# Kernel tuning notes

Hardware: AMD Instinct MI355X
Metric: run time of the kernel (lower is better)

## Reference

```python
import jax, jax.numpy as jnp
import numpy as np

B, NTH, NTW, M, DF = 64, 56, 56, 8, 8
FAR = 100.0  # sentinel location for off sources, as in the torch module


def setup_inputs() -> dict:
    key = jax.random.key(0)
    k1, k2, k3, k4, k5 = jax.random.split(key, 5)
    est_locs = jax.random.uniform(k1, (B, NTH, NTW, M, 2), dtype=jnp.float32)
    true_locs = jax.random.uniform(k2, (B, NTH, NTW, M, 2), dtype=jnp.float32)
    true_fluxes = jax.random.normal(k3, (B, NTH, NTW, M, DF), dtype=jnp.float32)
    est_n_sources = jax.random.randint(k4, (B, NTH, NTW), 0, M + 1, dtype=jnp.int32)
    true_n_sources = jax.random.randint(k5, (B, NTH, NTW), 0, M + 1, dtype=jnp.int32)
    return {"est_locs": est_locs, "true_locs": true_locs, "true_fluxes": true_fluxes,
            "est_n_sources": est_n_sources, "true_n_sources": true_n_sources}


def reference(est_locs, true_locs, true_fluxes, est_n_sources, true_n_sources):
    b, nth, ntw, m, _ = est_locs.shape
    T = b * nth * ntw
    slot = jnp.arange(m)
    # is_on_mask per tile: first n_sources slots are on
    est_on = slot[None, :] < est_n_sources.reshape(T, 1)    # [T, m] bool
    true_on = slot[None, :] < true_n_sources.reshape(T, 1)  # [T, m] bool

    # masked locs -> pairwise L2 distances (torch.cdist p=2)
    el = jnp.where(est_on[..., None], est_locs.reshape(T, m, 2), jnp.float32(FAR))
    tl = jnp.where(true_on[..., None], true_locs.reshape(T, m, 2), jnp.float32(FAR))
    diff = el[:, :, None, :] - tl[:, None, :, :]
    dist = jnp.sqrt(jnp.sum(diff * diff, axis=-1))  # [T, m, m]

    # _fast_one_to_one_match
    match1 = jnp.argmin(dist, axis=1)  # best est row per true col  [T, m]
    match2 = jnp.argmin(dist, axis=2)  # best true col per est row  [T, m]
    match1cond2 = jnp.take_along_axis(match1, match2, axis=1)
    one2one = match1cond2 == slot[None, :]
    est_out = match1 > (est_on.sum(-1, keepdims=True) - 1)
    true_out = match2 > (true_on.sum(-1, keepdims=True) - 1)
    one2one = one2one & ~(est_out | true_out)
    # unmatched pairs point to the padded dump slot m (== est_to_true*mask + offset)
    est_idx = jnp.where(one2one, match1, m)
    true_idx = jnp.where(one2one, match2, m)

    # flat indices across (b*nth*ntw) tiles, each of width m+1
    tile_off = (jnp.arange(T) * (m + 1))[:, None]
    flat_est = (est_idx + tile_off).reshape(-1)
    flat_true = (true_idx + tile_off).reshape(-1)

    # padded true catalog: locs(2) | fluxes(DF) | n_sources-indicator(1)
    fields = jnp.concatenate([
        true_locs.reshape(T, m, 2),
        true_fluxes.reshape(T, m, -1),
        true_on[..., None].astype(jnp.float32),
    ], axis=-1)  # [T, m, 2+DF+1]
    d = fields.shape[-1]
    padded = jnp.concatenate([fields, jnp.zeros((T, 1, d), fields.dtype)], axis=1)
    padded = padded.reshape(T * (m + 1), d)

    # gather matched true rows, scatter into est positions (zeros init)
    target = jnp.zeros_like(padded).at[flat_est].set(padded[flat_true])
    target = target.reshape(T, m + 1, d)[:, :m]  # drop dump slot (v[..., :-1, :])
    return target.reshape(b, nth, ntw, m, d)
```

## Files before the change

### kernel.cpp

```cpp
#include <hip/hip_runtime.h>
#include <math.h>

constexpr int TT = 64 * 56 * 56;

__global__ __launch_bounds__(256) void mvd_match_kernel(
    const float4* __restrict__ el4,
    const float*  __restrict__ tl,
    const float4* __restrict__ tf4,
    const int*    __restrict__ en_,
    const int*    __restrict__ tn_,
    float4*       __restrict__ out4)
{
#pragma clang fp contract(off)
    const int t = blockIdx.x * blockDim.x + threadIdx.x;
    if (t >= TT) return;

    const int en = en_[t];
    const int tn = tn_[t];

    const float4* tl4 = (const float4*)tl;
    float4 ea = el4[t * 4 + 0], eb = el4[t * 4 + 1];
    float4 ec = el4[t * 4 + 2], ed = el4[t * 4 + 3];
    float4 ta = tl4[t * 4 + 0], tb = tl4[t * 4 + 1];
    float4 tc = tl4[t * 4 + 2], td = tl4[t * 4 + 3];

    float mex[8], mey[8], mtx[8], mty[8];
    {
        const float exs[8] = {ea.x, ea.z, eb.x, eb.z, ec.x, ec.z, ed.x, ed.z};
        const float eys[8] = {ea.y, ea.w, eb.y, eb.w, ec.y, ec.w, ed.y, ed.w};
        const float txs[8] = {ta.x, ta.z, tb.x, tb.z, tc.x, tc.z, td.x, td.z};
        const float tys[8] = {ta.y, ta.w, tb.y, tb.w, tc.y, tc.w, td.y, td.w};
#pragma unroll
        for (int i = 0; i < 8; i++) {
            bool eon = i < en;
            bool ton = i < tn;
            mex[i] = eon ? exs[i] : 100.0f;
            mey[i] = eon ? eys[i] : 100.0f;
            mtx[i] = ton ? txs[i] : 100.0f;
            mty[i] = ton ? tys[i] : 100.0f;
        }
    }

    float colmin[8];
    int   m1[8];
    int   m2[8];
#pragma unroll
    for (int j = 0; j < 8; j++) { colmin[j] = 1e30f; m1[j] = 0; }
#pragma unroll
    for (int i = 0; i < 8; i++) {
        float rmin = 1e30f;
        int   rj = 0;
#pragma unroll
        for (int j = 0; j < 8; j++) {
            float dx = mex[i] - mtx[j];
            float dy = mey[i] - mty[j];
            float dx2 = dx * dx;
            float dy2 = dy * dy;
            float d = sqrtf(dx2 + dy2);
            if (d < rmin) { rmin = d; rj = j; }
            if (d < colmin[j]) { colmin[j] = d; m1[j] = i; }
        }
        m2[i] = rj;
    }

    int m1p = 0;
#pragma unroll
    for (int j = 0; j < 8; j++) m1p |= m1[j] << (3 * j);

    int rowsrc = 0;
#pragma unroll
    for (int k = 0; k < 8; k++) {
        int j = m2[k];
        int m1j = (m1p >> (3 * j)) & 7;
        bool o2o = (m1j == k) && (m1[k] < en) && (m2[k] < tn);
        if (o2o) {
            int r = m1[k];
            rowsrc = (rowsrc & ~(0xF << (4 * r))) | ((8 | j) << (4 * r));
        }
    }

    float o[88];
#pragma unroll
    for (int q = 0; q < 88; q++) o[q] = 0.0f;

    const float2* tl2 = (const float2*)tl;
#pragma unroll
    for (int r = 0; r < 8; r++) {
        int v = (rowsrc >> (4 * r)) & 15;
        if (v & 8) {
            int j = v & 7;
            float2 p  = tl2[t * 8 + j];
            float4 f0 = tf4[t * 16 + 2 * j];
            float4 f1 = tf4[t * 16 + 2 * j + 1];
            o[11 * r + 0] = p.x;
            o[11 * r + 1] = p.y;
            o[11 * r + 2] = f0.x; o[11 * r + 3] = f0.y;
            o[11 * r + 4] = f0.z; o[11 * r + 5] = f0.w;
            o[11 * r + 6] = f1.x; o[11 * r + 7] = f1.y;
            o[11 * r + 8] = f1.z; o[11 * r + 9] = f1.w;
            o[11 * r + 10] = (j < tn) ? 1.0f : 0.0f;
        }
    }

#pragma unroll
    for (int q = 0; q < 22; q++) {
        out4[t * 22 + q] = make_float4(o[4 * q + 0], o[4 * q + 1],
                                       o[4 * q + 2], o[4 * q + 3]);
    }
}

extern "C" void kernel_launch(void* const* d_in, const int* in_sizes, int n_in,
                              void* d_out, int out_size, void* d_ws, size_t ws_size,
                              hipStream_t stream) {
    const float* est_locs    = (const float*)d_in[0];
    const float* true_locs   = (const float*)d_in[1];
    const float* true_fluxes = (const float*)d_in[2];
    const int*   est_n       = (const int*)d_in[3];
    const int*   true_n      = (const int*)d_in[4];
    float* out = (float*)d_out;

    const int threads = 256;
    const int blocks = (TT + threads - 1) / threads;
    mvd_match_kernel<<<blocks, threads, 0, stream>>>(
        (const float4*)est_locs, true_locs, (const float4*)true_fluxes,
        est_n, true_n, (float4*)out);
}
```

Measured before the change: 154.1 us.

## Split matching and output write into two kernels for coalesced stores

Splits the per-tile kernel in two. The first computes the one-to-one match and stores a packed 32-bit row-source word per tile in workspace. The second launches one thread per output float4 so stores are fully coalesced instead of each thread writing 22 strided float4s, and reads the matched true locs and fluxes per element. The cost is an extra launch, a workspace round trip, and scalar gather loads. A monolithic fallback is kept for when the workspace is too small.

Result: no change. 151.4 us (-1.7%).

```diff
diff --git a/kernel.cpp b/kernel.cpp
--- a/kernel.cpp
+++ b/kernel.cpp
@@ -3,22 +3,19 @@
 
 constexpr int TT = 64 * 56 * 56;
 
-__global__ __launch_bounds__(256) void mvd_match_kernel(
+__global__ __launch_bounds__(256) void mvd_match_only(
     const float4* __restrict__ el4,
-    const float*  __restrict__ tl,
-    const float4* __restrict__ tf4,
+    const float4* __restrict__ tl4,
     const int*    __restrict__ en_,
     const int*    __restrict__ tn_,
-    float4*       __restrict__ out4)
+    int*          __restrict__ match)
 {
 #pragma clang fp contract(off)
     const int t = blockIdx.x * blockDim.x + threadIdx.x;
-    if (t >= TT) return;
 
     const int en = en_[t];
     const int tn = tn_[t];
 
-    const float4* tl4 = (const float4*)tl;
     float4 ea = el4[t * 4 + 0], eb = el4[t * 4 + 1];
     float4 ec = el4[t * 4 + 2], ed = el4[t * 4 + 3];
     float4 ta = tl4[t * 4 + 0], tb = tl4[t * 4 + 1];
@@ -42,8 +39,7 @@
     }
 
     float colmin[8];
-    int   m1[8];
-    int   m2[8];
+    int   m1[8], m2[8];
 #pragma unroll
     for (int j = 0; j < 8; j++) { colmin[j] = 1e30f; m1[j] = 0; }
 #pragma unroll
@@ -78,35 +74,109 @@
             rowsrc = (rowsrc & ~(0xF << (4 * r))) | ((8 | j) << (4 * r));
         }
     }
-
-    float o[88];
-#pragma unroll
-    for (int q = 0; q < 88; q++) o[q] = 0.0f;
-
-    const float2* tl2 = (const float2*)tl;
-#pragma unroll
-    for (int r = 0; r < 8; r++) {
-        int v = (rowsrc >> (4 * r)) & 15;
+    match[t] = rowsrc;
+}
+
+__global__ __launch_bounds__(256) void mvd_write(
+    const float*  __restrict__ tl,
+    const float*  __restrict__ tf,
+    const int*    __restrict__ match,
+    float4*       __restrict__ out4)
+{
+    const int idx = blockIdx.x * blockDim.x + threadIdx.x;
+    const int t = idx / 22;
+    const int q = idx - t * 22;
+    const int w = match[t];
+
+    float res[4];
+#pragma unroll
+    for (int u = 0; u < 4; u++) {
+        int p = 4 * q + u;
+        int r = (p * 94) >> 10;
+        int c = p - r * 11;
+        int v = (w >> (4 * r)) & 15;
+        float val = 0.0f;
         if (v & 8) {
             int j = v & 7;
-            float2 p  = tl2[t * 8 + j];
-            float4 f0 = tf4[t * 16 + 2 * j];
-            float4 f1 = tf4[t * 16 + 2 * j + 1];
-            o[11 * r + 0] = p.x;
-            o[11 * r + 1] = p.y;
-            o[11 * r + 2] = f0.x; o[11 * r + 3] = f0.y;
-            o[11 * r + 4] = f0.z; o[11 * r + 5] = f0.w;
-            o[11 * r + 6] = f1.x; o[11 * r + 7] = f1.y;
-            o[11 * r + 8] = f1.z; o[11 * r + 9] = f1.w;
-            o[11 * r + 10] = (j < tn) ? 1.0f : 0.0f;
-        }
-    }
-
-#pragma unroll
-    for (int q = 0; q < 22; q++) {
-        out4[t * 22 + q] = make_float4(o[4 * q + 0], o[4 * q + 1],
-                                       o[4 * q + 2], o[4 * q + 3]);
-    }
+            if (c == 10)      val = 1.0f;
+            else if (c < 2)   val = tl[(t << 4) + (j << 1) + c];
+            else              val = tf[(t << 6) + (j << 3) + (c - 2)];
+        }
+        res[u] = val;
+    }
+    out4[idx] = make_float4(res[0], res[1], res[2], res[3]);
+}
+
+__global__ __launch_bounds__(256) void mvd_mono(
+    const float4* __restrict__ el4, const float* __restrict__ tl,
+    const float4* __restrict__ tf4, const int* __restrict__ en_,
+    const int* __restrict__ tn_, float4* __restrict__ out4)
+{
+#pragma clang fp contract(off)
+    const int t = blockIdx.x * blockDim.x + threadIdx.x;
+    const int en = en_[t], tn = tn_[t];
+    const float4* tl4 = (const float4*)tl;
+    float4 ea = el4[t*4+0], eb = el4[t*4+1], ec = el4[t*4+2], ed = el4[t*4+3];
+    float4 ta = tl4[t*4+0], tb = tl4[t*4+1], tc = tl4[t*4+2], td = tl4[t*4+3];
+    float mex[8], mey[8], mtx[8], mty[8];
+    {
+        const float exs[8] = {ea.x,ea.z,eb.x,eb.z,ec.x,ec.z,ed.x,ed.z};
+        const float eys[8] = {ea.y,ea.w,eb.y,eb.w,ec.y,ec.w,ed.y,ed.w};
+        const float txs[8] = {ta.x,ta.z,tb.x,tb.z,tc.x,tc.z,td.x,td.z};
+        const float tys[8] = {ta.y,ta.w,tb.y,tb.w,tc.y,tc.w,td.y,td.w};
+#pragma unroll
+        for (int i = 0; i < 8; i++) {
+            mex[i] = (i < en) ? exs[i] : 100.0f;
+            mey[i] = (i < en) ? eys[i] : 100.0f;
+            mtx[i] = (i < tn) ? txs[i] : 100.0f;
+            mty[i] = (i < tn) ? tys[i] : 100.0f;
+        }
+    }
+    float colmin[8]; int m1[8], m2[8];
+#pragma unroll
+    for (int j = 0; j < 8; j++) { colmin[j] = 1e30f; m1[j] = 0; }
+#pragma unroll
+    for (int i = 0; i < 8; i++) {
+        float rmin = 1e30f; int rj = 0;
+#pragma unroll
+        for (int j = 0; j < 8; j++) {
+            float dx = mex[i]-mtx[j], dy = mey[i]-mty[j];
+            float d = sqrtf(dx*dx + dy*dy);
+            if (d < rmin) { rmin = d; rj = j; }
+            if (d < colmin[j]) { colmin[j] = d; m1[j] = i; }
+        }
+        m2[i] = rj;
+    }
+    int m1p = 0;
+#pragma unroll
+    for (int j = 0; j < 8; j++) m1p |= m1[j] << (3*j);
+    int rowsrc = 0;
+#pragma unroll
+    for (int k = 0; k < 8; k++) {
+        int j = m2[k];
+        bool o2o = (((m1p >> (3*j)) & 7) == k) && (m1[k] < en) && (m2[k] < tn);
+        if (o2o) rowsrc = (rowsrc & ~(0xF << (4*m1[k]))) | ((8|j) << (4*m1[k]));
+    }
+    float o[88];
+#pragma unroll
+    for (int q = 0; q < 88; q++) o[q] = 0.0f;
+    const float2* tl2 = (const float2*)tl;
+#pragma unroll
+    for (int r = 0; r < 8; r++) {
+        int v = (rowsrc >> (4*r)) & 15;
+        if (v & 8) {
+            int j = v & 7;
+            float2 p = tl2[t*8+j];
+            float4 f0 = tf4[t*16+2*j], f1 = tf4[t*16+2*j+1];
+            o[11*r+0]=p.x; o[11*r+1]=p.y;
+            o[11*r+2]=f0.x; o[11*r+3]=f0.y; o[11*r+4]=f0.z; o[11*r+5]=f0.w;
+            o[11*r+6]=f1.x; o[11*r+7]=f1.y; o[11*r+8]=f1.z; o[11*r+9]=f1.w;
+            o[11*r+10] = (j < tn) ? 1.0f : 0.0f;
+        }
+    }
+#pragma unroll
+    for (int q = 0; q < 22; q++)
+        out4[t*22+q] = make_float4(o[4*q], o[4*q+1], o[4*q+2], o[4*q+3]);
 }
 
 extern "C" void kernel_launch(void* const* d_in, const int* in_sizes, int n_in,
@@ -119,9 +189,16 @@
     const int*   true_n      = (const int*)d_in[4];
     float* out = (float*)d_out;
 
-    const int threads = 256;
-    const int blocks = (TT + threads - 1) / threads;
-    mvd_match_kernel<<<blocks, threads, 0, stream>>>(
-        (const float4*)est_locs, true_locs, (const float4*)true_fluxes,
-        est_n, true_n, (float4*)out);
-}
+    if (ws_size >= (size_t)TT * sizeof(int)) {
+        int* match = (int*)d_ws;
+        mvd_match_only<<<TT / 256, 256, 0, stream>>>(
+            (const float4*)est_locs, (const float4*)true_locs,
+            est_n, true_n, match);
+        mvd_write<<<(TT * 22) / 256, 256, 0, stream>>>(
+            true_locs, true_fluxes, match, (float4*)out);
+    } else {
+        mvd_mono<<<TT / 256, 256, 0, stream>>>(
+            (const float4*)est_locs, true_locs, (const float4*)true_fluxes,
+            est_n, true_n, (float4*)out);
+    }
+}
```

## Coalesce output writes via shared-memory match table and block-cooperative store loop

Applied to the files above, without the earlier changes.

Each thread still computes one tile's match, but it now writes the packed row-source word to shared memory. After a barrier, the block stores its contiguous output span cooperatively, so consecutive threads write consecutive float4s instead of each thread writing 22 strided float4s. Gathers of true locs and fluxes become scalar loads indexed per element. This trades per-element index math and uncoalesced scalar gathers for coalesced stores and fewer live registers. The bounds check is dropped, which is safe because TT divides evenly by 256.

Result: no change. 151.3 us (-1.8%).

```diff
diff --git a/kernel.cpp b/kernel.cpp
--- a/kernel.cpp
+++ b/kernel.cpp
@@ -2,110 +2,112 @@
 #include <math.h>
 
 constexpr int TT = 64 * 56 * 56;
-
-__global__ __launch_bounds__(256) void mvd_match_kernel(
+__global__ __launch_bounds__(256) void mvd_fused_dense(
     const float4* __restrict__ el4,
-    const float*  __restrict__ tl,
-    const float4* __restrict__ tf4,
+    const float4* __restrict__ tl4,
+    const float*  __restrict__ tf,
     const int*    __restrict__ en_,
     const int*    __restrict__ tn_,
     float4*       __restrict__ out4)
 {
 #pragma clang fp contract(off)
-    const int t = blockIdx.x * blockDim.x + threadIdx.x;
-    if (t >= TT) return;
+    const int t0 = blockIdx.x * 256;
+    const int t  = t0 + threadIdx.x;
 
-    const int en = en_[t];
-    const int tn = tn_[t];
+    __shared__ int s_rowsrc[256];
 
-    const float4* tl4 = (const float4*)tl;
-    float4 ea = el4[t * 4 + 0], eb = el4[t * 4 + 1];
-    float4 ec = el4[t * 4 + 2], ed = el4[t * 4 + 3];
-    float4 ta = tl4[t * 4 + 0], tb = tl4[t * 4 + 1];
-    float4 tc = tl4[t * 4 + 2], td = tl4[t * 4 + 3];
+    {
+        const int en = en_[t];
+        const int tn = tn_[t];
 
-    float mex[8], mey[8], mtx[8], mty[8];
-    {
-        const float exs[8] = {ea.x, ea.z, eb.x, eb.z, ec.x, ec.z, ed.x, ed.z};
-        const float eys[8] = {ea.y, ea.w, eb.y, eb.w, ec.y, ec.w, ed.y, ed.w};
-        const float txs[8] = {ta.x, ta.z, tb.x, tb.z, tc.x, tc.z, td.x, td.z};
-        const float tys[8] = {ta.y, ta.w, tb.y, tb.w, tc.y, tc.w, td.y, td.w};
+        float4 ea = el4[t * 4 + 0], eb = el4[t * 4 + 1];
+        float4 ec = el4[t * 4 + 2], ed = el4[t * 4 + 3];
+        float4 ta = tl4[t * 4 + 0], tb = tl4[t * 4 + 1];
+        float4 tc = tl4[t * 4 + 2], td = tl4[t * 4 + 3];
+
+        float mex[8], mey[8], mtx[8], mty[8];
+        {
+            const float exs[8] = {ea.x, ea.z, eb.x, eb.z, ec.x, ec.z, ed.x, ed.z};
+            const float eys[8] = {ea.y, ea.w, eb.y, eb.w, ec.y, ec.w, ed.y, ed.w};
+            const float txs[8] = {ta.x, ta.z, tb.x, tb.z, tc.x, tc.z, td.x, td.z};
+            const float tys[8] = {ta.y, ta.w, tb.y, tb.w, tc.y, tc.w, td.y, td.w};
+#pragma unroll
+            for (int i = 0; i < 8; i++) {
+                mex[i] = (i < en) ? exs[i] : 100.0f;
+                mey[i] = (i < en) ? eys[i] : 100.0f;
+                mtx[i] = (i < tn) ? txs[i] : 100.0f;
+                mty[i] = (i < tn) ? tys[i] : 100.0f;
+            }
+        }
+
+        float colmin[8];
+        int   m1[8], m2[8];
+#pragma unroll
+        for (int j = 0; j < 8; j++) { colmin[j] = 1e30f; m1[j] = 0; }
 #pragma unroll
         for (int i = 0; i < 8; i++) {
-            bool eon = i < en;
-            bool ton = i < tn;
-            mex[i] = eon ? exs[i] : 100.0f;
-            mey[i] = eon ? eys[i] : 100.0f;
-            mtx[i] = ton ? txs[i] : 100.0f;
-            mty[i] = ton ? tys[i] : 100.0f;
+            float rmin = 1e30f;
+            int   rj = 0;
+#pragma unroll
+            for (int j = 0; j < 8; j++) {
+                float dx = mex[i] - mtx[j];
+                float dy = mey[i] - mty[j];
+                float dx2 = dx * dx;
+                float dy2 = dy * dy;
+                float d = sqrtf(dx2 + dy2);
+                if (d < rmin) { rmin = d; rj = j; }
+                if (d < colmin[j]) { colmin[j] = d; m1[j] = i; }
+            }
+            m2[i] = rj;
         }
+
+        int m1p = 0;
+#pragma unroll
+        for (int j = 0; j < 8; j++) m1p |= m1[j] << (3 * j);
+
+        int rowsrc = 0;
+#pragma unroll
+        for (int k = 0; k < 8; k++) {
+            int j = m2[k];
+            int m1j = (m1p >> (3 * j)) & 7;
+            bool o2o = (m1j == k) && (m1[k] < en) && (m2[k] < tn);
+            if (o2o) {
+                int r = m1[k];
+                rowsrc = (rowsrc & ~(0xF << (4 * r))) | ((8 | j) << (4 * r));
+            }
+        }
+        s_rowsrc[threadIdx.x] = rowsrc;
     }
+    __syncthreads();
 
-    float colmin[8];
-    int   m1[8];
-    int   m2[8];
-#pragma unroll
-    for (int j = 0; j < 8; j++) { colmin[j] = 1e30f; m1[j] = 0; }
-#pragma unroll
-    for (int i = 0; i < 8; i++) {
-        float rmin = 1e30f;
-        int   rj = 0;
-#pragma unroll
-        for (int j = 0; j < 8; j++) {
-            float dx = mex[i] - mtx[j];
-            float dy = mey[i] - mty[j];
-            float dx2 = dx * dx;
-            float dy2 = dy * dy;
-            float d = sqrtf(dx2 + dy2);
-            if (d < rmin) { rmin = d; rj = j; }
-            if (d < colmin[j]) { colmin[j] = d; m1[j] = i; }
-        }
-        m2[i] = rj;
-    }
-
-    int m1p = 0;
-#pragma unroll
-    for (int j = 0; j < 8; j++) m1p |= m1[j] << (3 * j);
-
-    int rowsrc = 0;
-#pragma unroll
-    for (int k = 0; k < 8; k++) {
-        int j = m2[k];
-        int m1j = (m1p >> (3 * j)) & 7;
-        bool o2o = (m1j == k) && (m1[k] < en) && (m2[k] < tn);
-        if (o2o) {
-            int r = m1[k];
-            rowsrc = (rowsrc & ~(0xF << (4 * r))) | ((8 | j) << (4 * r));
-        }
-    }
-
-    float o[88];
-#pragma unroll
-    for (int q = 0; q < 88; q++) o[q] = 0.0f;
-
-    const float2* tl2 = (const float2*)tl;
-#pragma unroll
-    for (int r = 0; r < 8; r++) {
-        int v = (rowsrc >> (4 * r)) & 15;
-        if (v & 8) {
-            int j = v & 7;
-            float2 p  = tl2[t * 8 + j];
-            float4 f0 = tf4[t * 16 + 2 * j];
-            float4 f1 = tf4[t * 16 + 2 * j + 1];
-            o[11 * r + 0] = p.x;
-            o[11 * r + 1] = p.y;
-            o[11 * r + 2] = f0.x; o[11 * r + 3] = f0.y;
-            o[11 * r + 4] = f0.z; o[11 * r + 5] = f0.w;
-            o[11 * r + 6] = f1.x; o[11 * r + 7] = f1.y;
-            o[11 * r + 8] = f1.z; o[11 * r + 9] = f1.w;
-            o[11 * r + 10] = (j < tn) ? 1.0f : 0.0f;
-        }
-    }
+    const float* tl = (const float*)tl4;
+    float4* oblk = out4 + (size_t)t0 * 22;
 
 #pragma unroll
-    for (int q = 0; q < 22; q++) {
-        out4[t * 22 + q] = make_float4(o[4 * q + 0], o[4 * q + 1],
-                                       o[4 * q + 2], o[4 * q + 3]);
+    for (int it = 0; it < 22; it++) {
+        const int i  = threadIdx.x + it * 256;
+        const int tl_ = i / 22;
+        const int q  = i - tl_ * 22;
+        const int w  = s_rowsrc[tl_];
+        const int tt = t0 + tl_;
+
+        float res[4];
+#pragma unroll
+        for (int u = 0; u < 4; u++) {
+            int p = 4 * q + u;
+            int r = (p * 94) >> 10;
+            int c = p - r * 11;
+            int v = (w >> (4 * r)) & 15;
+            float val = 0.0f;
+            if (v & 8) {
+                int j = v & 7;
+                if (c == 10)      val = 1.0f;
+                else if (c < 2)   val = tl[(tt << 4) + (j << 1) + c];
+                else              val = tf[(tt << 6) + (j << 3) + (c - 2)];
+            }
+            res[u] = val;
+        }
+        oblk[i] = make_float4(res[0], res[1], res[2], res[3]);
     }
 }
 
@@ -119,9 +121,7 @@
     const int*   true_n      = (const int*)d_in[4];
     float* out = (float*)d_out;
 
-    const int threads = 256;
-    const int blocks = (TT + threads - 1) / threads;
-    mvd_match_kernel<<<blocks, threads, 0, stream>>>(
-        (const float4*)est_locs, true_locs, (const float4*)true_fluxes,
+    mvd_fused_dense<<<TT / 256, 256, 0, stream>>>(
+        (const float4*)est_locs, (const float4*)true_locs, true_fluxes,
         est_n, true_n, (float4*)out);
 }
```
